# Performance work log

Hardware: AMD Instinct MI355X
Metric: run time of the kernel (lower is better)

The kernel has to match this reference:

```python
import jax, jax.numpy as jnp
import numpy as np

NUM_USERS = 200_000
NUM_ITEMS = 60_000
NUM_NODES = NUM_USERS + NUM_ITEMS          # 260_000
NUM_UI_EDGES = 2_500_000
EMBED_DIM = 64
K = 4
ALPHA = 0.1
BETA = 0.9


def setup_inputs() -> dict:
    key = jax.random.key(0)
    kx, = jax.random.split(key, 1)
    rng = np.random.default_rng(0)
    u = rng.integers(0, NUM_USERS, NUM_UI_EDGES).astype(np.int32)
    i = (rng.integers(0, NUM_ITEMS, NUM_UI_EDGES) + NUM_USERS).astype(np.int32)
    loops = np.arange(NUM_NODES, dtype=np.int32)
    # homo graph: forward user->item, reverse item->user, self loops
    src = np.concatenate([u, i, loops])
    dst = np.concatenate([i, u, loops])
    x = jax.random.normal(kx, (NUM_NODES, EMBED_DIM), dtype=jnp.float32)
    return {"x": x, "src": jnp.asarray(src), "dst": jnp.asarray(dst)}


def reference(x, src, dst):
    N, D = x.shape
    # symmetric normalization: deg^-0.5[src] * deg^-0.5[dst] (in-degree; graph is symmetric)
    deg = jax.ops.segment_sum(jnp.ones(src.shape, dtype=x.dtype), dst, num_segments=N)
    inv_sqrt = jnp.where(deg > 0, jax.lax.rsqrt(jnp.maximum(deg, 1.0)), 0.0)
    norm = inv_sqrt[src] * inv_sqrt[dst]  # [E]

    gamma = BETA ** K + ALPHA * sum(BETA ** i for i in range(K))

    h0 = x  # x_dropout is identity at eval (rate 0)
    h = h0
    for _ in range(K):  # small fixed k, not a data dim
        # SpMM: h_new[n] = sum_{e: dst[e]==n} norm[e] * h[src[e]]
        msg = h[src] * norm[:, None]                       # [E, D]
        agg = jax.ops.segment_sum(msg, dst, num_segments=N)
        h = agg * BETA + h0 * ALPHA
    return h / gamma  # z_dropout identity at eval
```

## Files before the change

kernel.cpp:

```cpp
#include <hip/hip_runtime.h>

#define NUM_USERS 200000
#define NUM_ITEMS 60000
#define NUM_NODES 260000
#define EMBED_DIM 64
#define ALPHA 0.1f
#define BETA 0.9f

static constexpr int SCAN_BLOCK = 256;
static constexpr int NCHUNKS = (NUM_NODES + SCAN_BLOCK - 1) / SCAN_BLOCK;



__global__ void degree_kernel(const int* __restrict__ u_arr, const int* __restrict__ i_arr,
                              int* __restrict__ deg, int E_ui) {
    int stride = gridDim.x * blockDim.x;
    for (int e = blockIdx.x * blockDim.x + threadIdx.x; e < E_ui; e += stride) {
        atomicAdd(&deg[i_arr[e]], 1);
        atomicAdd(&deg[u_arr[e]], 1);
    }
}

__global__ void block_sum_kernel(const int* __restrict__ deg, int* __restrict__ partials) {
    int i = blockIdx.x * SCAN_BLOCK + threadIdx.x;
    int v = (i < NUM_NODES) ? deg[i] : 0;
    for (int off = 32; off > 0; off >>= 1) v += __shfl_down(v, off, 64);
    __shared__ int s[4];
    int wave = threadIdx.x >> 6, lane = threadIdx.x & 63;
    if (lane == 0) s[wave] = v;
    __syncthreads();
    if (threadIdx.x == 0) partials[blockIdx.x] = s[0] + s[1] + s[2] + s[3];
}

__global__ void scan_partials_kernel(int* __restrict__ partials, int n) {
    __shared__ int tmp[1024];
    int t = threadIdx.x;
    tmp[t] = (t < n) ? partials[t] : 0;
    __syncthreads();
    for (int off = 1; off < 1024; off <<= 1) {
        int add = (t >= off) ? tmp[t - off] : 0;
        __syncthreads();
        tmp[t] += add;
        __syncthreads();
    }
    if (t < n) partials[t] = (t == 0) ? 0 : tmp[t - 1];
}

__global__ void scan_final_kernel(const int* __restrict__ deg, const int* __restrict__ partials,
                                  int* __restrict__ row_ptr, int* __restrict__ cursor,
                                  float* __restrict__ inv_sqrt, int csr_E) {
    __shared__ int tmp[SCAN_BLOCK];
    int chunk = blockIdx.x, t = threadIdx.x;
    int i = chunk * SCAN_BLOCK + t;
    int v = (i < NUM_NODES) ? deg[i] : 0;
    tmp[t] = v;
    __syncthreads();
    for (int off = 1; off < SCAN_BLOCK; off <<= 1) {
        int add = (t >= off) ? tmp[t - off] : 0;
        __syncthreads();
        tmp[t] += add;
        __syncthreads();
    }
    int excl = tmp[t] - v;
    if (i < NUM_NODES) {
        int rp = partials[chunk] + excl;
        row_ptr[i] = rp;
        cursor[i]  = rp;
        inv_sqrt[i] = rsqrtf((float)(v + 1));
    }
    if (i == 0) row_ptr[NUM_NODES] = csr_E;
}

__global__ void scatter_kernel(const int* __restrict__ u_arr, const int* __restrict__ i_arr,
                               int* __restrict__ cursor, int* __restrict__ csr_src, int E_ui) {
    int stride = gridDim.x * blockDim.x;
    for (int e = blockIdx.x * blockDim.x + threadIdx.x; e < E_ui; e += stride) {
        int u = u_arr[e], it = i_arr[e];
        int p0 = atomicAdd(&cursor[it], 1);
        csr_src[p0] = u;
        int p1 = atomicAdd(&cursor[u], 1);
        csr_src[p1] = it;
    }
}


__global__ __launch_bounds__(256) void spmm_kernel(const float* __restrict__ h,
                                                   const float* __restrict__ x,
                                                   const int* __restrict__ row_ptr,
                                                   const int* __restrict__ csr_src,
                                                   const float* __restrict__ inv_sqrt,
                                                   float* __restrict__ out) {
    int node = (blockIdx.x << 2) + (threadIdx.x >> 6);
    if (node >= NUM_NODES) return;
    int lane = threadIdx.x & 63;
    int q    = lane >> 4;
    int dpos = lane & 15;
    int begin = row_ptr[node];
    int end   = row_ptr[node + 1];

    float4 accA = {0.f, 0.f, 0.f, 0.f};
    float4 accB = {0.f, 0.f, 0.f, 0.f};

    int j = begin;
    for (; j + 8 <= end; j += 8) {
        int e0 = j + q, e1 = j + 4 + q;
        int   s0 = csr_src[e0],   s1 = csr_src[e1];
        float w0 = inv_sqrt[s0],  w1 = inv_sqrt[s1];
        const float4 v0 = *(const float4*)(h + (size_t)s0 * EMBED_DIM + (dpos << 2));
        const float4 v1 = *(const float4*)(h + (size_t)s1 * EMBED_DIM + (dpos << 2));
        accA.x = fmaf(w0, v0.x, accA.x);
        accA.y = fmaf(w0, v0.y, accA.y);
        accA.z = fmaf(w0, v0.z, accA.z);
        accA.w = fmaf(w0, v0.w, accA.w);
        accB.x = fmaf(w1, v1.x, accB.x);
        accB.y = fmaf(w1, v1.y, accB.y);
        accB.z = fmaf(w1, v1.z, accB.z);
        accB.w = fmaf(w1, v1.w, accB.w);
    }
    if (j + 4 <= end) {
        int e = j + q;
        int s = csr_src[e];
        float w = inv_sqrt[s];
        const float4 v = *(const float4*)(h + (size_t)s * EMBED_DIM + (dpos << 2));
        accA.x = fmaf(w, v.x, accA.x);
        accA.y = fmaf(w, v.y, accA.y);
        accA.z = fmaf(w, v.z, accA.z);
        accA.w = fmaf(w, v.w, accA.w);
        j += 4;
    }
    int rem = end - j;
    if (q < rem) {
        int s = csr_src[j + q];
        float w = inv_sqrt[s];
        const float4 v = *(const float4*)(h + (size_t)s * EMBED_DIM + (dpos << 2));
        accB.x = fmaf(w, v.x, accB.x);
        accB.y = fmaf(w, v.y, accB.y);
        accB.z = fmaf(w, v.z, accB.z);
        accB.w = fmaf(w, v.w, accB.w);
    }
    accA.x += accB.x; accA.y += accB.y; accA.z += accB.z; accA.w += accB.w;
    accA.x += __shfl_xor(accA.x, 16, 64);
    accA.y += __shfl_xor(accA.y, 16, 64);
    accA.z += __shfl_xor(accA.z, 16, 64);
    accA.w += __shfl_xor(accA.w, 16, 64);
    accA.x += __shfl_xor(accA.x, 32, 64);
    accA.y += __shfl_xor(accA.y, 32, 64);
    accA.z += __shfl_xor(accA.z, 32, 64);
    accA.w += __shfl_xor(accA.w, 32, 64);

    if (q == 0) {
        float is   = inv_sqrt[node];
        size_t o   = (size_t)node * EMBED_DIM + (dpos << 2);
        const float4 hv = *(const float4*)(h + o);
        const float4 xv = *(const float4*)(x + o);
        accA.x = fmaf(is, hv.x, accA.x);
        accA.y = fmaf(is, hv.y, accA.y);
        accA.z = fmaf(is, hv.z, accA.z);
        accA.w = fmaf(is, hv.w, accA.w);
        float scale = BETA * is;
        float4 r;
        r.x = fmaf(accA.x, scale, ALPHA * xv.x);
        r.y = fmaf(accA.y, scale, ALPHA * xv.y);
        r.z = fmaf(accA.z, scale, ALPHA * xv.z);
        r.w = fmaf(accA.w, scale, ALPHA * xv.w);
        *(float4*)(out + o) = r;
    }
}


extern "C" void kernel_launch(void* const* d_in, const int* in_sizes, int n_in,
                              void* d_out, int out_size, void* d_ws, size_t ws_size,
                              hipStream_t stream) {
    const float* x   = (const float*)d_in[0];
    const int*   src = (const int*)d_in[1];
    const int*   dst = (const int*)d_in[2];
    const int    E   = in_sizes[1];
    const int    E_ui  = (E - NUM_NODES) / 2;
    const int    csr_E = 2 * E_ui;
    float* out = (float*)d_out;

    const int* u_arr = src;
    const int* i_arr = dst;

    char* ws = (char*)d_ws;
    size_t off = 0;
    auto alloc = [&](size_t bytes) -> void* {
        void* p = ws + off;
        off = (off + bytes + 255) & ~(size_t)255;
        return p;
    };
    int*   deg      = (int*)alloc((size_t)NUM_NODES * 4);
    int*   cursor   = (int*)alloc((size_t)NUM_NODES * 4);
    float* inv_sqrt = (float*)alloc((size_t)NUM_NODES * 4);
    int*   row_ptr  = (int*)alloc((size_t)(NUM_NODES + 1) * 4);
    int*   partials = (int*)alloc((size_t)NCHUNKS * 4);
    int*   csr_src  = (int*)alloc((size_t)csr_E * 4);
    float* hA       = (float*)alloc((size_t)NUM_NODES * EMBED_DIM * 4);

    hipMemsetAsync(deg, 0, (size_t)NUM_NODES * 4, stream);

    degree_kernel<<<2048, 256, 0, stream>>>(u_arr, i_arr, deg, E_ui);
    block_sum_kernel<<<NCHUNKS, SCAN_BLOCK, 0, stream>>>(deg, partials);
    scan_partials_kernel<<<1, 1024, 0, stream>>>(partials, NCHUNKS);
    scan_final_kernel<<<NCHUNKS, SCAN_BLOCK, 0, stream>>>(deg, partials, row_ptr, cursor,
                                                          inv_sqrt, csr_E);
    scatter_kernel<<<4096, 256, 0, stream>>>(u_arr, i_arr, cursor, csr_src, E_ui);

    const int nblocks = (NUM_NODES + 3) / 4;
    spmm_kernel<<<nblocks, 256, 0, stream>>>(x,   x, row_ptr, csr_src, inv_sqrt, hA);
    spmm_kernel<<<nblocks, 256, 0, stream>>>(hA,  x, row_ptr, csr_src, inv_sqrt, out);
    spmm_kernel<<<nblocks, 256, 0, stream>>>(out, x, row_ptr, csr_src, inv_sqrt, hA);
    spmm_kernel<<<nblocks, 256, 0, stream>>>(hA,  x, row_ptr, csr_src, inv_sqrt, out);
}
```

Measured before the change: 1.520 ms.

## Build CSR via two-level bucketed binning with shared-memory cursors

Replaces the global-atomic scatter that builds the CSR with a two-pass bucket sort. Edges are first binned into 24 node-range buckets using per-block LDS histograms and a scan. A per-bucket kernel then places the packed entries into final CSR slots using LDS cursor atomics. This aims to cut random global atomics and scattered writes, but adds several launches and an extra edge array pass, and the placement step runs on only 24 blocks.

```diff
diff --git a/kernel.cpp b/kernel.cpp
--- a/kernel.cpp
+++ b/kernel.cpp
@@ -6,6 +6,15 @@
 #define EMBED_DIM 64
 #define ALPHA 0.1f
 #define BETA 0.9f
+
+#define N_UBKT 16
+#define UB_SZ  12500
+#define N_IBKT 8
+#define IB_SZ  7500
+#define NBKT   (N_UBKT + N_IBKT)
+
+#define NBLK_BIN 1024
+#define BIN_THREADS 256
 
 static constexpr int SCAN_BLOCK = 256;
 static constexpr int NCHUNKS = (NUM_NODES + SCAN_BLOCK - 1) / SCAN_BLOCK;
@@ -47,8 +56,8 @@
 }
 
 __global__ void scan_final_kernel(const int* __restrict__ deg, const int* __restrict__ partials,
-                                  int* __restrict__ row_ptr, int* __restrict__ cursor,
-                                  float* __restrict__ inv_sqrt, int csr_E) {
+                                  int* __restrict__ row_ptr, float* __restrict__ inv_sqrt,
+                                  int csr_E) {
     __shared__ int tmp[SCAN_BLOCK];
     int chunk = blockIdx.x, t = threadIdx.x;
     int i = chunk * SCAN_BLOCK + t;
@@ -63,26 +72,100 @@
     }
     int excl = tmp[t] - v;
     if (i < NUM_NODES) {
-        int rp = partials[chunk] + excl;
-        row_ptr[i] = rp;
-        cursor[i]  = rp;
+        row_ptr[i] = partials[chunk] + excl;
         inv_sqrt[i] = rsqrtf((float)(v + 1));
     }
     if (i == 0) row_ptr[NUM_NODES] = csr_E;
 }
 
-__global__ void scatter_kernel(const int* __restrict__ u_arr, const int* __restrict__ i_arr,
-                               int* __restrict__ cursor, int* __restrict__ csr_src, int E_ui) {
+
+__global__ __launch_bounds__(BIN_THREADS) void count_kernel(const int* __restrict__ u_arr,
+                                                            const int* __restrict__ i_arr,
+                                                            int* __restrict__ blkcnt, int E_ui) {
+    __shared__ int hist[NBKT];
+    if (threadIdx.x < NBKT) hist[threadIdx.x] = 0;
+    __syncthreads();
     int stride = gridDim.x * blockDim.x;
     for (int e = blockIdx.x * blockDim.x + threadIdx.x; e < E_ui; e += stride) {
-        int u = u_arr[e], it = i_arr[e];
-        int p0 = atomicAdd(&cursor[it], 1);
-        csr_src[p0] = u;
-        int p1 = atomicAdd(&cursor[u], 1);
-        csr_src[p1] = it;
-    }
-}
-
+        int u  = u_arr[e];
+        int il = i_arr[e] - NUM_USERS;
+        atomicAdd(&hist[N_UBKT + il / IB_SZ], 1);
+        atomicAdd(&hist[u / UB_SZ], 1);
+    }
+    __syncthreads();
+    if (threadIdx.x < NBKT)
+        blkcnt[threadIdx.x * NBLK_BIN + blockIdx.x] = hist[threadIdx.x];
+}
+
+__global__ __launch_bounds__(NBLK_BIN) void scan_bkt_kernel(const int* __restrict__ row_ptr,
+                                                            const int* __restrict__ blkcnt,
+                                                            int* __restrict__ blk_base) {
+    __shared__ int tmp[NBLK_BIN];
+    int b = blockIdx.x, t = threadIdx.x;
+    int v = blkcnt[b * NBLK_BIN + t];
+    tmp[t] = v;
+    __syncthreads();
+    for (int off = 1; off < NBLK_BIN; off <<= 1) {
+        int add = (t >= off) ? tmp[t - off] : 0;
+        __syncthreads();
+        tmp[t] += add;
+        __syncthreads();
+    }
+    int node_base = (b < N_UBKT) ? b * UB_SZ : NUM_USERS + (b - N_UBKT) * IB_SZ;
+    blk_base[b * NBLK_BIN + t] = row_ptr[node_base] + (tmp[t] - v);
+}
+
+__global__ __launch_bounds__(BIN_THREADS) void bin_kernel(const int* __restrict__ u_arr,
+                                                          const int* __restrict__ i_arr,
+                                                          const int* __restrict__ blk_base,
+                                                          unsigned int* __restrict__ binned,
+                                                          int E_ui) {
+    __shared__ int cur[NBKT];
+    if (threadIdx.x < NBKT)
+        cur[threadIdx.x] = blk_base[threadIdx.x * NBLK_BIN + blockIdx.x];
+    __syncthreads();
+    int stride = gridDim.x * blockDim.x;
+    for (int e = blockIdx.x * blockDim.x + threadIdx.x; e < E_ui; e += stride) {
+        int u  = u_arr[e];
+        int it = i_arr[e];
+        int il = it - NUM_USERS;
+        int ib = il / IB_SZ;
+        int ub = u / UB_SZ;
+        int p0 = atomicAdd(&cur[N_UBKT + ib], 1);
+        binned[p0] = ((unsigned)(il - ib * IB_SZ) << 18) | (unsigned)u;
+        int p1 = atomicAdd(&cur[ub], 1);
+        binned[p1] = ((unsigned)(u - ub * UB_SZ) << 16) | (unsigned)il;
+    }
+}
+
+#define PLACE_THREADS 1024
+__global__ __launch_bounds__(PLACE_THREADS) void place_kernel(const int* __restrict__ row_ptr,
+                                                              const unsigned int* __restrict__ binned,
+                                                              int* __restrict__ csr_src) {
+    __shared__ int cur[UB_SZ];
+    int b = blockIdx.x;
+    bool user_b = (b < N_UBKT);
+    int node_base = user_b ? b * UB_SZ : NUM_USERS + (b - N_UBKT) * IB_SZ;
+    int ncnt      = user_b ? UB_SZ : IB_SZ;
+    for (int i = threadIdx.x; i < ncnt; i += PLACE_THREADS)
+        cur[i] = row_ptr[node_base + i];
+    __syncthreads();
+    int beg = row_ptr[node_base];
+    int end = row_ptr[node_base + ncnt];
+    if (user_b) {
+        for (int j = beg + (int)threadIdx.x; j < end; j += PLACE_THREADS) {
+            unsigned int v = binned[j];
+            int p = atomicAdd(&cur[v >> 16], 1);
+            csr_src[p] = (int)(v & 0xFFFF) + NUM_USERS;
+        }
+    } else {
+        for (int j = beg + (int)threadIdx.x; j < end; j += PLACE_THREADS) {
+            unsigned int v = binned[j];
+            int p = atomicAdd(&cur[v >> 18], 1);
+            csr_src[p] = (int)(v & 0x3FFFF);
+        }
+    }
+}
 
 __global__ __launch_bounds__(256) void spmm_kernel(const float* __restrict__ h,
                                                    const float* __restrict__ x,
@@ -118,8 +201,7 @@
         accB.w = fmaf(w1, v1.w, accB.w);
     }
     if (j + 4 <= end) {
-        int e = j + q;
-        int s = csr_src[e];
+        int s = csr_src[j + q];
         float w = inv_sqrt[s];
         const float4 v = *(const float4*)(h + (size_t)s * EMBED_DIM + (dpos << 2));
         accA.x = fmaf(w, v.x, accA.x);
@@ -189,22 +271,27 @@
         off = (off + bytes + 255) & ~(size_t)255;
         return p;
     };
-    int*   deg      = (int*)alloc((size_t)NUM_NODES * 4);
-    int*   cursor   = (int*)alloc((size_t)NUM_NODES * 4);
-    float* inv_sqrt = (float*)alloc((size_t)NUM_NODES * 4);
-    int*   row_ptr  = (int*)alloc((size_t)(NUM_NODES + 1) * 4);
-    int*   partials = (int*)alloc((size_t)NCHUNKS * 4);
-    int*   csr_src  = (int*)alloc((size_t)csr_E * 4);
-    float* hA       = (float*)alloc((size_t)NUM_NODES * EMBED_DIM * 4);
+    int*          deg      = (int*)alloc((size_t)NUM_NODES * 4);
+    float*        inv_sqrt = (float*)alloc((size_t)NUM_NODES * 4);
+    int*          row_ptr  = (int*)alloc((size_t)(NUM_NODES + 1) * 4);
+    int*          partials = (int*)alloc((size_t)NCHUNKS * 4);
+    int*          blkcnt   = (int*)alloc((size_t)NBKT * NBLK_BIN * 4);
+    int*          blk_base = (int*)alloc((size_t)NBKT * NBLK_BIN * 4);
+    unsigned int* binned   = (unsigned int*)alloc((size_t)csr_E * 4);
+    int*          csr_src  = (int*)alloc((size_t)csr_E * 4);
+    float*        hA       = (float*)alloc((size_t)NUM_NODES * EMBED_DIM * 4);
 
     hipMemsetAsync(deg, 0, (size_t)NUM_NODES * 4, stream);
 
     degree_kernel<<<2048, 256, 0, stream>>>(u_arr, i_arr, deg, E_ui);
     block_sum_kernel<<<NCHUNKS, SCAN_BLOCK, 0, stream>>>(deg, partials);
     scan_partials_kernel<<<1, 1024, 0, stream>>>(partials, NCHUNKS);
-    scan_final_kernel<<<NCHUNKS, SCAN_BLOCK, 0, stream>>>(deg, partials, row_ptr, cursor,
+    scan_final_kernel<<<NCHUNKS, SCAN_BLOCK, 0, stream>>>(deg, partials, row_ptr,
                                                           inv_sqrt, csr_E);
-    scatter_kernel<<<4096, 256, 0, stream>>>(u_arr, i_arr, cursor, csr_src, E_ui);
+    count_kernel<<<NBLK_BIN, BIN_THREADS, 0, stream>>>(u_arr, i_arr, blkcnt, E_ui);
+    scan_bkt_kernel<<<NBKT, NBLK_BIN, 0, stream>>>(row_ptr, blkcnt, blk_base);
+    bin_kernel<<<NBLK_BIN, BIN_THREADS, 0, stream>>>(u_arr, i_arr, blk_base, binned, E_ui);
+    place_kernel<<<NBKT, PLACE_THREADS, 0, stream>>>(row_ptr, binned, csr_src);
 
     const int nblocks = (NUM_NODES + 3) / 4;
     spmm_kernel<<<nblocks, 256, 0, stream>>>(x,   x, row_ptr, csr_src, inv_sqrt, hA);
```

Result: faster. 1.434 ms (-5.7%).
